# Optimization experiments

Hardware: AMD Instinct MI355X
Metric: run time of the kernel (lower is better)

## Reference

```python
import jax, jax.numpy as jnp
import numpy as np

B, T, D = 32, 200, 256
H, DH = 4, 32
INNER = H * DH  # 128
L, FF, NI = 8, 1024, 100000
NB = 64  # gap/recency buckets


def _ln(x, g, b, eps=1e-5):
    m = x.mean(-1, keepdims=True)
    v = jnp.mean((x - m) ** 2, -1, keepdims=True)
    return (x - m) / jnp.sqrt(v + eps) * g + b


def _gelu(x):
    return jax.nn.gelu(x, approximate=False)


def _dwconv_causal(x, w, b):
    # x: [B,T,C], w: [C,k] depthwise kernel, causal left-pad (k-1)
    k = w.shape[1]
    xp = jnp.pad(x, ((0, 0), (k - 1, 0), (0, 0))).transpose(0, 2, 1)  # [B,C,T+k-1]
    out = jax.lax.conv_general_dilated(
        xp, w[:, None, :], (1,), 'VALID',
        dimension_numbers=('NCH', 'OIH', 'NCH'), feature_group_count=w.shape[0])
    return out.transpose(0, 2, 1) + b


def _causal_linear_attention(q, k, v, m4):
    q = (jax.nn.elu(q) + 1.0) * m4
    k = (jax.nn.elu(k) + 1.0) * m4
    v = v * m4
    kv = jnp.einsum('bthd,bthe->bthde', k, v)          # [B,T,H,DH,DH]
    kv_prefix = jnp.cumsum(kv, axis=1)
    k_prefix = jnp.cumsum(k, axis=1)
    num = jnp.einsum('bthd,bthde->bthe', q, kv_prefix)
    den = jnp.sum(q * k_prefix, -1, keepdims=True)
    return num / (den + 1e-6) * m4


def _forward(item_emb, pos_emb, gap_emb, rec_emb, tf_w1, tf_b1, tf_w2, tf_b2,
             in_g, in_b, l_ln1g, l_ln1b, l_win, l_bin, l_wc, l_bc, l_tw, l_tb,
             l_pw, l_pb, l_wmix, l_bmix, l_ln2g, l_ln2b, l_wf1, l_bf1, l_wf2, l_bf2,
             fn_g, fn_b, pg_w, pg_b, uh_w1, uh_b1, uh_lng, uh_lnb, uh_w2, uh_b2,
             item_bias, ids, ts, lens):
    Bb, Tt = ids.shape
    pos = jnp.arange(Tt)
    mask = pos[None, :] >= (Tt - lens)[:, None]  # right-aligned valid mask [B,T]
    prev_ts = jnp.roll(ts, 1, axis=1)
    prev_mask = jnp.roll(mask, 1, axis=1).at[:, 0].set(False)
    zero = jnp.zeros_like(ts)
    gap_vals = jnp.where(mask & prev_mask, jnp.maximum(ts - prev_ts, 0), zero)
    latest = ts[:, -1:]
    rec_vals = jnp.where(mask, jnp.maximum(latest - ts, 0), zero)

    def buck(v, n):
        vf = jnp.maximum(v.astype(jnp.float32), 0.0)
        return jnp.clip(jnp.floor(jnp.log2(vf + 1.0)), 0, n - 1).astype(jnp.int32)

    gb = buck(gap_vals, NB)
    rb = buck(rec_vals, NB)
    rec_raw = jnp.maximum(latest - ts, 0).astype(jnp.float32)
    tf = jnp.stack([jnp.log1p(gb.astype(jnp.float32)), jnp.log1p(rec_raw)], -1)  # [B,T,2]
    dense_time = _gelu(tf @ tf_w1 + tf_b1) @ tf_w2 + tf_b2

    x = item_emb[ids] + pos_emb[None] + gap_emb[gb] + rec_emb[rb] + dense_time
    mf = mask[..., None].astype(x.dtype)
    m4 = mask[..., None, None].astype(x.dtype)
    x = _ln(x, in_g, in_b) * mf

    for i in range(L):
        res = x
        nrm = _ln(x, l_ln1g[i], l_ln1b[i])
        proj = nrm @ l_win[i] + l_bin[i]  # [B,T,D+3*INNER]
        gate = proj[..., :D]
        q = proj[..., D:D + INNER].reshape(Bb, Tt, H, DH)
        k = proj[..., D + INNER:D + 2 * INNER].reshape(Bb, Tt, H, DH)
        v = proj[..., D + 2 * INNER:].reshape(Bb, Tt, H, DH)
        content = _causal_linear_attention(q, k, v, m4).reshape(Bb, Tt, INNER) @ l_wc[i] + l_bc[i]
        temporal = _dwconv_causal(nrm, l_tw[i], l_tb[i])
        positional = _dwconv_causal(nrm, l_pw[i], l_pb[i])
        mixed = jnp.concatenate([content, temporal, positional], -1) @ l_wmix[i] + l_bmix[i]
        x = (res + jax.nn.sigmoid(gate) * mixed) * mf
        h = _ln(x, l_ln2g[i], l_ln2b[i])
        ffn = _gelu(h @ l_wf1[i] + l_bf1[i]) @ l_wf2[i] + l_bf2[i]
        x = (x + ffn) * mf

    x = _ln(x, fn_g, fn_b) * mf
    denom = jnp.maximum(lens, 1)[:, None].astype(x.dtype)
    mean_pooled = (x * mf).sum(1) / denom
    ps = (x @ pg_w + pg_b)[..., 0]
    ps = jnp.where(mask, ps, -1e9)
    pw = jax.nn.softmax(ps, axis=1)[..., None]
    attn_pooled = (pw * x).sum(1)
    last = x[:, -1, :]
    u = jnp.concatenate([last, mean_pooled, attn_pooled], -1)
    u = _gelu(u @ uh_w1 + uh_b1)
    u = _ln(u, uh_lng, uh_lnb)
    u = u @ uh_w2 + uh_b2
    u = u / jnp.maximum(jnp.linalg.norm(u, axis=-1, keepdims=True), 1e-12)
    ie = item_emb[1:]
    ie = ie / jnp.maximum(jnp.linalg.norm(ie, axis=-1, keepdims=True), 1e-12)
    return u @ ie.T + item_bias[1:]


def setup_inputs() -> dict:
    key = jax.random.key(0)
    it = iter(jax.random.split(key, 64))
    def nk():
        return next(it)
    def w(*s):
        return jax.random.normal(nk(), s, jnp.float32) * 0.02
    inp = dict(
        history_ids=jax.random.randint(nk(), (B, T), 0, NI),
        history_timestamps=jnp.sort(jax.random.randint(nk(), (B, T), 0, 1000000), axis=1),
        history_lengths=jax.random.randint(nk(), (B,), 1, T + 1),
        item_emb=w(NI + 1, D).at[0].set(0.0),
        pos_emb=w(T, D), gap_emb=w(NB, D), rec_emb=w(NB, D),
        tf_w1=w(2, D), tf_b1=jnp.zeros((D,)), tf_w2=w(D, D), tf_b2=jnp.zeros((D,)),
        in_g=jnp.ones((D,)), in_b=jnp.zeros((D,)),
        l_ln1g=jnp.ones((L, D)), l_ln1b=jnp.zeros((L, D)),
        l_win=w(L, D, D + 3 * INNER), l_bin=jnp.zeros((L, D + 3 * INNER)),
        l_wc=w(L, INNER, D), l_bc=jnp.zeros((L, D)),
        l_tw=w(L, D, 3), l_tb=jnp.zeros((L, D)),
        l_pw=w(L, D, 5), l_pb=jnp.zeros((L, D)),
        l_wmix=w(L, 3 * D, D), l_bmix=jnp.zeros((L, D)),
        l_ln2g=jnp.ones((L, D)), l_ln2b=jnp.zeros((L, D)),
        l_wf1=w(L, D, FF), l_bf1=jnp.zeros((L, FF)),
        l_wf2=w(L, FF, D), l_bf2=jnp.zeros((L, D)),
        fn_g=jnp.ones((D,)), fn_b=jnp.zeros((D,)),
        pg_w=w(D, 1), pg_b=jnp.zeros((1,)),
        uh_w1=w(3 * D, 1024), uh_b1=jnp.zeros((1024,)),
        uh_lng=jnp.ones((1024,)), uh_lnb=jnp.zeros((1024,)),
        uh_w2=w(1024, D), uh_b2=jnp.zeros((D,)),
        item_bias=jnp.zeros((NI + 1,)),
    )
    return inp


def reference(history_ids, history_timestamps, history_lengths, item_emb, pos_emb,
              gap_emb, rec_emb, tf_w1, tf_b1, tf_w2, tf_b2, in_g, in_b, l_ln1g,
              l_ln1b, l_win, l_bin, l_wc, l_bc, l_tw, l_tb, l_pw, l_pb, l_wmix,
              l_bmix, l_ln2g, l_ln2b, l_wf1, l_bf1, l_wf2, l_bf2, fn_g, fn_b,
              pg_w, pg_b, uh_w1, uh_b1, uh_lng, uh_lnb, uh_w2, uh_b2, item_bias):
    return _forward(item_emb, pos_emb, gap_emb, rec_emb, tf_w1, tf_b1, tf_w2, tf_b2,
                    in_g, in_b, l_ln1g, l_ln1b, l_win, l_bin, l_wc, l_bc, l_tw, l_tb,
                    l_pw, l_pb, l_wmix, l_bmix, l_ln2g, l_ln2b, l_wf1, l_bf1, l_wf2,
                    l_bf2, fn_g, fn_b, pg_w, pg_b, uh_w1, uh_b1, uh_lng, uh_lnb,
                    uh_w2, uh_b2, item_bias, history_ids, history_timestamps,
                    history_lengths)
```

## Files before the change

kernel.cpp:

```cpp
#include <hip/hip_runtime.h>
#include <math.h>

#define B_ 32
#define T_ 200
#define D_ 256
#define H_ 4
#define DH_ 32
#define INNER_ 128
#define L_ 8
#define FF_ 1024
#define NI_ 100000
#define NB_ 64
#define CH_ 25

typedef __attribute__((ext_vector_type(8))) short short8;
typedef __attribute__((ext_vector_type(8))) unsigned short ushort8;
typedef __attribute__((ext_vector_type(4))) unsigned short ushort4v;
typedef __attribute__((ext_vector_type(4))) float floatx4;

__device__ __forceinline__ float gelu_f(float x){
  return 0.5f*x*(1.0f+erff(x*0.70710678118654752f));
}
__device__ __forceinline__ float wsum(float v){
  #pragma unroll
  for (int o=32;o>0;o>>=1) v += __shfl_xor(v,o,64);
  return v;
}
__device__ __forceinline__ unsigned short f2bf(float x){
  unsigned int u = __float_as_uint(x);
  unsigned int r = (u + 0x7fffu + ((u>>16)&1u)) >> 16;
  return (unsigned short)r;
}
__device__ __forceinline__ float bf2f(unsigned short u){
  return __uint_as_float(((unsigned int)u)<<16);
}

__device__ __forceinline__ void cvt_tile(const float* __restrict__ src, unsigned short* __restrict__ dst,
                                         int K, int N, int tk, int tn, int tid, float (*s)[33])
{
  int tx = tid & 31, ty0 = tid >> 5;
  #pragma unroll
  for (int it=0; it<4; ++it){
    int ty = ty0 + it*8;
    s[ty][tx] = src[(size_t)(tk*32+ty)*N + tn*32+tx];
  }
  __syncthreads();
  #pragma unroll
  for (int it=0; it<4; ++it){
    int ty = ty0 + it*8;
    dst[(size_t)(tn*32+ty)*K + tk*32 + tx] = f2bf(s[tx][ty]);
  }
}

__global__ __launch_bounds__(256) void k_cvtAll(
  const float* __restrict__ win, const float* __restrict__ wmix,
  const float* __restrict__ wf1, const float* __restrict__ wf2,
  const float* __restrict__ tfw2, const float* __restrict__ uhw1, const float* __restrict__ uhw2,
  unsigned short* __restrict__ WtPerm, unsigned short* __restrict__ WtMixT,
  unsigned short* __restrict__ WtH)
{
  __shared__ float s[32][33];
  int b = blockIdx.x, tid = threadIdx.x;
  if (b < 6912){
    int l = b / 864, r = b % 864;
    if (r < 160)      cvt_tile(win + (size_t)l*163840, WtPerm + (size_t)l*688128,          256, 640,  r/20,      r%20,      tid, s);
    else if (r < 352){int t=r-160; cvt_tile(wmix + (size_t)l*196608, WtMixT + (size_t)l*196608, 768, 256, t/8, t%8, tid, s);}
    else if (r < 608){int t=r-352; cvt_tile(wf1 + (size_t)l*262144, WtPerm + (size_t)l*688128 + 163840, 256, 1024, t/32, t%32, tid, s);}
    else             {int t=r-608; cvt_tile(wf2 + (size_t)l*262144, WtPerm + (size_t)l*688128 + 425984, 1024, 256, t/8, t%8, tid, s);}
  } else {
    int r = b - 6912;
    if (r < 64)       cvt_tile(tfw2, WtH,        256, 256,  r/8,  r%8,  tid, s);
    else if (r < 832){int t=r-64;  cvt_tile(uhw1, WtH+65536,  768, 1024, t/32, t%32, tid, s);}
    else             {int t=r-832; cvt_tile(uhw2, WtH+851968, 1024, 256, t/8,  t%8,  tid, s);}
  }
}

__global__ __launch_bounds__(256) void k_asm(
  const float* __restrict__ WcombF, const unsigned short* __restrict__ WtMixT,
  unsigned short* __restrict__ WtBig)
{
  int l = blockIdx.x >> 3, g = blockIdx.x & 7;
  int tid = threadIdx.x;
  int n = g*32 + (tid >> 3);
  int k0 = (tid & 7) * 80;
  const float* wc = WcombF + (size_t)l*32768;
  const unsigned short* wm = WtMixT + (size_t)l*196608 + (size_t)n*768;
  unsigned short* dst = WtBig + (size_t)l*163840 + (size_t)n*640;
  for (int kk=0; kk<80; kk++){
    int k = k0 + kk;
    dst[k] = (k < 128) ? f2bf(wc[(size_t)k*256 + n]) : wm[k+128];
  }
}

__global__ __launch_bounds__(256) void k_bfold(
  const float* __restrict__ bc, const float* __restrict__ bmix,
  const float* __restrict__ wmix, float* __restrict__ bmixP)
{
  int l = blockIdx.x; int n = threadIdx.x;
  const float* w = wmix + (size_t)l*196608;
  const float* c = bc + l*256;
  float s = bmix[l*256 + n];
  for (int d=0; d<256; d++) s += c[d]*w[(size_t)d*256 + n];
  bmixP[l*256+n] = s;
}

template<int TN>
__global__ __launch_bounds__(256) void k_gemm_bf(
    const float* __restrict__ A, const unsigned short* __restrict__ Wt,
    const float* __restrict__ bias, float* __restrict__ C,
    int M, int N, int K, int ldA, int ldW, int ldC, int mode,
    size_t sA, size_t sW, size_t sC, size_t sB)
{
  constexpr int NJ = TN/32;
  __shared__ unsigned short Als[128][40];
  __shared__ unsigned short Bls[TN][40];
  int z = blockIdx.z;
  A += (size_t)z*sA; Wt += (size_t)z*sW; C += (size_t)z*sC;
  const float* bz = bias ? bias + (size_t)z*sB : nullptr;
  int tid = threadIdx.x;
  int wave = tid >> 6, lane = tid & 63;
  int wm = (wave >> 1) * 64, wn = (wave & 1) * (TN/2);
  int frow = lane & 15, kg = lane >> 4;
  int bm = blockIdx.y * 128, bn = blockIdx.x * TN;
  int sm = tid >> 1, skh = (tid & 1) * 16;

  floatx4 acc[4][NJ];
  #pragma unroll
  for (int i=0;i<4;i++)
    #pragma unroll
    for (int j=0;j<NJ;j++) acc[i][j] = (floatx4){0.f,0.f,0.f,0.f};

  for (int k0=0; k0<K; k0+=32){
    {
      int gm = bm + sm;
      float f[16];
      if (gm < M){
        const float4* ap = (const float4*)(A + (size_t)gm*ldA + k0 + skh);
        #pragma unroll
        for (int c=0;c<4;c++){ float4 v = ap[c]; f[c*4]=v.x; f[c*4+1]=v.y; f[c*4+2]=v.z; f[c*4+3]=v.w; }
      } else {
        #pragma unroll
        for (int c=0;c<16;c++) f[c]=0.f;
      }
      ushort8 pa, pb;
      #pragma unroll
      for (int c=0;c<8;c++){ pa[c]=f2bf(f[c]); pb[c]=f2bf(f[8+c]); }
      *(ushort8*)&Als[sm][skh]   = pa;
      *(ushort8*)&Als[sm][skh+8] = pb;
    }
    #pragma unroll
    for (int u=0; u<TN/64; u++){
      int li = tid + u*256;
      int row = li >> 2, koff = (li & 3) * 8;
      int gn = bn + row;
      ushort8 wv;
      if (gn < N){
        wv = *(const ushort8*)&Wt[(size_t)gn*ldW + k0 + koff];
      } else {
        for (int c=0;c<8;c++) wv[c]=0;
      }
      *(ushort8*)&Bls[row][koff] = wv;
    }
    __syncthreads();
    short8 af[4], bf[NJ];
    #pragma unroll
    for (int i=0;i<4;i++) af[i] = *(const short8*)&Als[wm + 16*i + frow][kg*8];
    #pragma unroll
    for (int j=0;j<NJ;j++) bf[j] = *(const short8*)&Bls[wn + 16*j + frow][kg*8];
    #pragma unroll
    for (int i=0;i<4;i++)
      #pragma unroll
      for (int j=0;j<NJ;j++)
        acc[i][j] = __builtin_amdgcn_mfma_f32_16x16x32_bf16(af[i], bf[j], acc[i][j], 0, 0, 0);
    __syncthreads();
  }

  #pragma unroll
  for (int j=0;j<NJ;j++){
    int n = bn + wn + 16*j + frow;
    float bv = bz ? bz[n] : 0.f;
    #pragma unroll
    for (int i=0;i<4;i++){
      int m0 = bm + wm + 16*i + kg*4;
      #pragma unroll
      for (int r=0;r<4;r++){
        int m = m0 + r;
        if (m < M){
          float v = acc[i][j][r] + bv;
          if (mode == 1) v = gelu_f(v);
          float* cp = &C[(size_t)m*ldC + n];
          if (mode == 2) v += *cp;
          *cp = v;
        }
      }
    }
  }
}

template<int K>
__global__ __launch_bounds__(256) void k_gemm16(
    const unsigned short* __restrict__ A, const unsigned short* __restrict__ Wt,
    const float* __restrict__ bias, void* __restrict__ Cv,
    int ldA, int ldW, int ldC, int mode)
{
  int tid = threadIdx.x;
  int wave = tid >> 6, lane = tid & 63;
  int frow = lane & 15, kg = lane >> 4;
  int bm = blockIdx.y * 32;
  int bn = blockIdx.x * 128 + wave * 32;

  const unsigned short* a0 = A + (size_t)(bm + frow)*ldA + kg*8;
  const unsigned short* a1 = a0 + (size_t)16*ldA;
  const unsigned short* b0 = Wt + (size_t)(bn + frow)*ldW + kg*8;
  const unsigned short* b1 = b0 + (size_t)16*ldW;

  floatx4 acc[2][2];
  #pragma unroll
  for (int i=0;i<2;i++)
    #pragma unroll
    for (int j=0;j<2;j++) acc[i][j] = (floatx4){0.f,0.f,0.f,0.f};

  #pragma unroll
  for (int k0=0; k0<K; k0+=32){
    short8 af0 = *(const short8*)(a0 + k0);
    short8 af1 = *(const short8*)(a1 + k0);
    short8 bf0 = *(const short8*)(b0 + k0);
    short8 bf1 = *(const short8*)(b1 + k0);
    acc[0][0] = __builtin_amdgcn_mfma_f32_16x16x32_bf16(af0, bf0, acc[0][0], 0, 0, 0);
    acc[0][1] = __builtin_amdgcn_mfma_f32_16x16x32_bf16(af0, bf1, acc[0][1], 0, 0, 0);
    acc[1][0] = __builtin_amdgcn_mfma_f32_16x16x32_bf16(af1, bf0, acc[1][0], 0, 0, 0);
    acc[1][1] = __builtin_amdgcn_mfma_f32_16x16x32_bf16(af1, bf1, acc[1][1], 0, 0, 0);
  }

  float* Cf = (float*)Cv;
  unsigned short* Ch = (unsigned short*)Cv;
  #pragma unroll
  for (int j=0;j<2;j++){
    int n = bn + 16*j + frow;
    float bv = bias[n];
    #pragma unroll
    for (int i=0;i<2;i++){
      int m0 = bm + 16*i + kg*4;
      #pragma unroll
      for (int r=0;r<4;r++){
        float v = acc[i][j][r] + bv;
        size_t off = (size_t)(m0+r)*ldC + n;
        if (mode == 1)      Cf[off] = gelu_f(v);
        else if (mode == 2) Cf[off] += v;
        else if (mode == 4) Ch[off] = f2bf(gelu_f(v));
        else                Cf[off] = v;
      }
    }
  }
}

__global__ __launch_bounds__(256) void k_embed(
  const int* __restrict__ ids, const int* __restrict__ ts, const int* __restrict__ lens,
  const float* __restrict__ item_emb, const float* __restrict__ pos_emb,
  const float* __restrict__ gap_emb, const float* __restrict__ rec_emb,
  const float* __restrict__ tf_w1, const float* __restrict__ tf_b1,
  float* __restrict__ xbuf, unsigned short* __restrict__ tfh)
{
  int bt = blockIdx.x;
  int b = bt / T_, t = bt % T_;
  int d = threadIdx.x;
  int len = lens[b];
  int tcur = ts[b*T_+t];
  int tlast = ts[b*T_+T_-1];
  bool mask  = t >= T_ - len;
  bool pmask = (t >= 1) && ((t-1) >= T_ - len);
  int gap = 0;
  if (mask && pmask){ int pv = ts[b*T_+t-1]; gap = max(tcur - pv, 0); }
  int rec = mask ? max(tlast - tcur, 0) : 0;
  int gb = min(max((int)floorf(log2f((float)gap + 1.0f)), 0), NB_-1);
  int rb = min(max((int)floorf(log2f((float)rec + 1.0f)), 0), NB_-1);
  float rec_raw = (float)max(tlast - tcur, 0);
  float tf0 = log1pf((float)gb);
  float tf1 = log1pf(rec_raw);
  float hid = gelu_f(tf0*tf_w1[d] + tf1*tf_w1[D_+d] + tf_b1[d]);
  tfh[(size_t)bt*D_ + d] = f2bf(hid);
  int id = ids[b*T_+t];
  xbuf[(size_t)bt*D_ + d] = item_emb[(size_t)id*D_ + d] + pos_emb[t*D_ + d]
                          + gap_emb[gb*D_ + d] + rec_emb[rb*D_ + d];
}

template<int NC>
__global__ __launch_bounds__(256) void k_ln(
  const float* __restrict__ in, void* __restrict__ out,
  const float* __restrict__ g, const float* __restrict__ bb,
  int rows, const int* __restrict__ lens, int applyMask, int outBf)
{
  int wid = threadIdx.x >> 6, lane = threadIdx.x & 63;
  int r = blockIdx.x*4 + wid;
  if (r >= rows) return;
  const int D = NC*256;
  const float4* rp = (const float4*)(in + (size_t)r*D);
  float4 v[NC];
  float s = 0.f;
  #pragma unroll
  for (int c=0;c<NC;c++){ v[c] = rp[c*64 + lane]; s += v[c].x+v[c].y+v[c].z+v[c].w; }
  s = wsum(s);
  float mean = s / (float)D;
  float q = 0.f;
  #pragma unroll
  for (int c=0;c<NC;c++){
    float a=v[c].x-mean, b2=v[c].y-mean, c2=v[c].z-mean, d2=v[c].w-mean;
    q += a*a + b2*b2 + c2*c2 + d2*d2;
  }
  q = wsum(q);
  float rstd = rsqrtf(q/(float)D + 1e-5f);
  float m = 1.f;
  if (applyMask){ int t = r % T_; int b = r / T_; m = (t >= T_ - lens[b]) ? 1.f : 0.f; }
  #pragma unroll
  for (int c=0;c<NC;c++){
    float4 gg  = ((const float4*)g )[c*64+lane];
    float4 bv  = ((const float4*)bb)[c*64+lane];
    float4 o;
    o.x = ((v[c].x-mean)*rstd*gg.x + bv.x)*m;
    o.y = ((v[c].y-mean)*rstd*gg.y + bv.y)*m;
    o.z = ((v[c].z-mean)*rstd*gg.z + bv.z)*m;
    o.w = ((v[c].w-mean)*rstd*gg.w + bv.w)*m;
    if (outBf){
      ushort4v ob; ob.x=f2bf(o.x); ob.y=f2bf(o.y); ob.z=f2bf(o.z); ob.w=f2bf(o.w);
      ((ushort4v*)((unsigned short*)out + (size_t)r*D))[c*64+lane] = ob;
    } else {
      ((float4*)((float*)out + (size_t)r*D))[c*64+lane] = o;
    }
  }
}

__global__ __launch_bounds__(256) void k_lnln(
  float* __restrict__ x, const int* __restrict__ lens,
  const float* __restrict__ g1, const float* __restrict__ b1,
  const float* __restrict__ g2, const float* __restrict__ b2,
  unsigned short* __restrict__ nrm)
{
  int wid = threadIdx.x >> 6, lane = threadIdx.x & 63;
  int r = blockIdx.x*4 + wid;
  int t = r % T_, b = r / T_;
  float m = (t >= T_ - lens[b]) ? 1.f : 0.f;
  float4 v = ((const float4*)(x + (size_t)r*256))[lane];
  float s = wsum(v.x+v.y+v.z+v.w);
  float mean = s/256.f;
  float a=v.x-mean, b2v=v.y-mean, c2=v.z-mean, d2=v.w-mean;
  float q = wsum(a*a+b2v*b2v+c2*c2+d2*d2);
  float rstd = rsqrtf(q/256.f + 1e-5f);
  float4 gg = ((const float4*)g1)[lane];
  float4 bv = ((const float4*)b1)[lane];
  float4 xn;
  xn.x = (a*rstd*gg.x + bv.x)*m;
  xn.y = (b2v*rstd*gg.y + bv.y)*m;
  xn.z = (c2*rstd*gg.z + bv.z)*m;
  xn.w = (d2*rstd*gg.w + bv.w)*m;
  ((float4*)(x + (size_t)r*256))[lane] = xn;
  float s2 = wsum(xn.x+xn.y+xn.z+xn.w);
  float mean2 = s2/256.f;
  float a2=xn.x-mean2, b22=xn.y-mean2, c22=xn.z-mean2, d22=xn.w-mean2;
  float q2 = wsum(a2*a2+b22*b22+c22*c22+d22*d22);
  float rstd2 = rsqrtf(q2/256.f + 1e-5f);
  float4 gg2 = ((const float4*)g2)[lane];
  float4 bv2 = ((const float4*)b2)[lane];
  ushort4v o;
  o.x = f2bf(a2*rstd2*gg2.x + bv2.x);
  o.y = f2bf(b22*rstd2*gg2.y + bv2.y);
  o.z = f2bf(c22*rstd2*gg2.z + bv2.z);
  o.w = f2bf(d22*rstd2*gg2.w + bv2.w);
  ((ushort4v*)(nrm + (size_t)r*256))[lane] = o;
}

__global__ __launch_bounds__(64) void k_attn_sums(
  const float* __restrict__ proj, const int* __restrict__ lens, float* __restrict__ Ssum)
{
  int blk = blockIdx.x;
  int bh = blk >> 3, c = blk & 7;
  int b = bh >> 2, h = bh & 3;
  int lane = threadIdx.x; int e = lane & 31, half = lane >> 5;
  int tstart = T_ - lens[b];
  __shared__ float sk[CH_*32], sv[CH_*32];
  int t0 = c*CH_;
  for (int idx = lane; idx < CH_*32; idx += 64){
    int tl = idx >> 5, dd = idx & 31;
    int t = t0 + tl;
    float m = (t >= tstart) ? 1.f : 0.f;
    const float* pr = proj + (size_t)(b*T_+t)*640 + h*32 + dd;
    float kw = pr[384], vv = pr[512];
    sk[idx] = (kw > 0.f ? kw + 1.f : __expf(kw)) * m;
    sv[idx] = vv * m;
  }
  __syncthreads();
  float acc[16];
  #pragma unroll
  for (int j=0;j<16;j++) acc[j]=0.f;
  for (int tl=0; tl<CH_; tl++){
    const float4* k4 = (const float4*)(sk + tl*32 + half*16);
    float vf = sv[tl*32 + e];
    #pragma unroll
    for (int jj=0;jj<4;jj++){
      float4 kk = k4[jj];
      acc[jj*4+0] += kk.x*vf;
      acc[jj*4+1] += kk.y*vf;
      acc[jj*4+2] += kk.z*vf;
      acc[jj*4+3] += kk.w*vf;
    }
  }
  float* dst = Ssum + ((size_t)bh*8 + c)*1056;
  #pragma unroll
  for (int j=0;j<16;j++) dst[(half*16+j)*32 + e] = acc[j];
  if (half == 0){
    float s = 0.f;
    for (int tl=0; tl<CH_; tl++) s += sk[tl*32 + e];
    dst[1024 + e] = s;
  }
}

__global__ __launch_bounds__(256) void k_dwpfx(
  const unsigned short* __restrict__ nrm, const float* __restrict__ tw, const float* __restrict__ tb,
  const float* __restrict__ pw, const float* __restrict__ pb, unsigned short* __restrict__ cat,
  float* __restrict__ Ssum)
{
  int bid = blockIdx.x;
  if (bid < 6400){
    int idx = bid*256 + threadIdx.x;
    int d = idx & 255; int bt = idx >> 8; int t = bt % T_;
    float xs[5];
    #pragma unroll
    for (int j=0;j<5;j++){
      int tt = t - 4 + j;
      xs[j] = (tt >= 0) ? bf2f(nrm[(size_t)(bt - 4 + j)*D_ + d]) : 0.f;
    }
    float tmp = tw[d*3+0]*xs[2] + tw[d*3+1]*xs[3] + tw[d*3+2]*xs[4] + tb[d];
    float pos = pb[d];
    #pragma unroll
    for (int j=0;j<5;j++) pos += pw[d*5+j]*xs[j];
    cat[(size_t)bt*640 + 128 + d] = f2bf(tmp);
    cat[(size_t)bt*640 + 384 + d] = f2bf(pos);
  } else {
    int idx = (bid - 6400)*256 + threadIdx.x;
    int bh = idx / 1056, r = idx - bh*1056;
    float* p = Ssum + (size_t)bh*8*1056 + r;
    float s = p[0];
    #pragma unroll
    for (int c=1;c<8;c++){ s += p[(size_t)c*1056]; p[(size_t)c*1056] = s; }
  }
}

__global__ __launch_bounds__(128) void k_attn_out(
  const float* __restrict__ proj, const int* __restrict__ lens,
  const float* __restrict__ Ssum, unsigned short* __restrict__ cat)
{
  int blk = blockIdx.x;
  int bh = blk >> 3, c = blk & 7;
  int b = bh >> 2, h = bh & 3;
  int tid = threadIdx.x; int e = tid & 31, qg = tid >> 5;
  int tstart = T_ - lens[b];
  __shared__ float sq[CH_*32], sk[CH_*32], sv[CH_*32];
  __shared__ float P[1056];
  __shared__ float A[CH_][CH_+1];
  __shared__ float sden[CH_];
  int t0 = c*CH_;
  if (c > 0){
    const float* Pp = Ssum + ((size_t)bh*8 + (c-1))*1056;
    for (int idx = tid; idx < 1056; idx += 128) P[idx] = Pp[idx];
  } else {
    for (int idx = tid; idx < 1056; idx += 128) P[idx] = 0.f;
  }
  for (int idx = tid; idx < CH_*32; idx += 128){
    int tl = idx >> 5, dd = idx & 31;
    int t = t0 + tl;
    float m = (t >= tstart) ? 1.f : 0.f;
    const float* pr = proj + (size_t)(b*T_+t)*640 + h*32 + dd;
    float qv = pr[256], kw = pr[384], vv = pr[512];
    sq[idx] = (qv > 0.f ? qv + 1.f : __expf(qv)) * m;
    sk[idx] = (kw > 0.f ? kw + 1.f : __expf(kw)) * m;
    sv[idx] = vv * m;
  }
  __syncthreads();
  for (int idx = tid; idx < CH_*CH_; idx += 128){
    int t = idx / CH_, tp = idx - t*CH_;
    float s = 0.f;
    if (tp <= t){
      const float4* q4 = (const float4*)(sq + t*32);
      const float4* k4 = (const float4*)(sk + tp*32);
      #pragma unroll
      for (int jj=0;jj<8;jj++){
        float4 qq = q4[jj], kk = k4[jj];
        s += qq.x*kk.x + qq.y*kk.y + qq.z*kk.z + qq.w*kk.w;
      }
    }
    A[t][tp] = s;
  }
  __syncthreads();
  if (tid < CH_){
    int t = tid;
    float s = 0.f;
    for (int tp=0; tp<=t; tp++) s += A[t][tp];
    const float* qf = sq + t*32;
    #pragma unroll
    for (int d=0; d<32; d++) s += qf[d]*P[1024+d];
    sden[t] = s;
  }
  __syncthreads();
  int tlo = (qg*CH_) >> 2, thi = ((qg+1)*CH_) >> 2;
  for (int t = tlo; t < thi; t++){
    float num = 0.f;
    for (int tp=0; tp<=t; tp++) num += A[t][tp]*sv[tp*32+e];
    const float* qf = sq + t*32;
    #pragma unroll
    for (int d=0; d<32; d++) num += qf[d]*P[d*32+e];
    int tg = t0 + t;
    float m = (tg >= tstart) ? 1.f : 0.f;
    cat[(size_t)(b*T_+tg)*640 + h*32 + e] = f2bf(num/(sden[t]+1e-6f)*m);
  }
}

__global__ __launch_bounds__(256) void k_postmix_ln(
  float* __restrict__ x, const float* __restrict__ proj, const float* __restrict__ mixed,
  const int* __restrict__ lens, const float* __restrict__ g, const float* __restrict__ bb,
  unsigned short* __restrict__ h)
{
  int wid = threadIdx.x >> 6, lane = threadIdx.x & 63;
  int r = blockIdx.x*4 + wid;
  int t = r % T_, b = r / T_;
  float m = (t >= T_ - lens[b]) ? 1.f : 0.f;
  float4 xv = ((const float4*)(x     + (size_t)r*256))[lane];
  float4 gv = ((const float4*)(proj  + (size_t)r*640))[lane];
  float4 mx = ((const float4*)(mixed + (size_t)r*256))[lane];
  float4 xn;
  xn.x = (xv.x + mx.x/(1.f+__expf(-gv.x)))*m;
  xn.y = (xv.y + mx.y/(1.f+__expf(-gv.y)))*m;
  xn.z = (xv.z + mx.z/(1.f+__expf(-gv.z)))*m;
  xn.w = (xv.w + mx.w/(1.f+__expf(-gv.w)))*m;
  float s = wsum(xn.x+xn.y+xn.z+xn.w);
  float mean = s/256.f;
  float a=xn.x-mean, b2=xn.y-mean, c2=xn.z-mean, d2=xn.w-mean;
  float q = wsum(a*a+b2*b2+c2*c2+d2*d2);
  float rstd = rsqrtf(q/256.f + 1e-5f);
  ((float4*)(x + (size_t)r*256))[lane] = xn;
  float4 gg = ((const float4*)g )[lane];
  float4 bv = ((const float4*)bb)[lane];
  ushort4v o;
  o.x = f2bf(a*rstd*gg.x + bv.x);
  o.y = f2bf(b2*rstd*gg.y + bv.y);
  o.z = f2bf(c2*rstd*gg.z + bv.z);
  o.w = f2bf(d2*rstd*gg.w + bv.w);
  ((ushort4v*)(h + (size_t)r*256))[lane] = o;
}

__global__ __launch_bounds__(256) void k_addln(
  float* __restrict__ x, const float* __restrict__ f, const int* __restrict__ lens,
  const float* __restrict__ g, const float* __restrict__ bb,
  unsigned short* __restrict__ nrm, int maskLN)
{
  int wid = threadIdx.x >> 6, lane = threadIdx.x & 63;
  int r = blockIdx.x*4 + wid;
  int t = r % T_, b = r / T_;
  float m = (t >= T_ - lens[b]) ? 1.f : 0.f;
  float4 xv = ((const float4*)(x + (size_t)r*256))[lane];
  float4 fv = ((const float4*)(f + (size_t)r*256))[lane];
  float4 xn;
  xn.x = (xv.x + fv.x)*m;
  xn.y = (xv.y + fv.y)*m;
  xn.z = (xv.z + fv.z)*m;
  xn.w = (xv.w + fv.w)*m;
  float s = wsum(xn.x+xn.y+xn.z+xn.w);
  float mean = s/256.f;
  float a=xn.x-mean, b2=xn.y-mean, c2=xn.z-mean, d2=xn.w-mean;
  float q = wsum(a*a+b2*b2+c2*c2+d2*d2);
  float rstd = rsqrtf(q/256.f + 1e-5f);
  ((float4*)(x + (size_t)r*256))[lane] = xn;
  float ml = maskLN ? m : 1.f;
  float4 gg = ((const float4*)g )[lane];
  float4 bv = ((const float4*)bb)[lane];
  ushort4v o;
  o.x = f2bf((a*rstd*gg.x + bv.x)*ml);
  o.y = f2bf((b2*rstd*gg.y + bv.y)*ml);
  o.z = f2bf((c2*rstd*gg.z + bv.z)*ml);
  o.w = f2bf((d2*rstd*gg.w + bv.w)*ml);
  ((ushort4v*)(nrm + (size_t)r*256))[lane] = o;
}

__global__ __launch_bounds__(256) void k_pool(
  const unsigned short* __restrict__ x, const int* __restrict__ lens,
  const float* __restrict__ pg_w, const float* __restrict__ pg_b,
  float* __restrict__ u0)
{
  int b = blockIdx.x;
  int tid = threadIdx.x, wid = tid>>6, lane = tid&63;
  __shared__ float sps[T_];
  __shared__ float spw[T_];
  int len = lens[b]; int tstart = T_ - len;
  const float4* pw4 = (const float4*)pg_w;
  float4 wv = pw4[lane];
  for (int t = wid; t < T_; t += 4){
    ushort4v xv = ((const ushort4v*)(x + (size_t)(b*T_+t)*D_))[lane];
    float dot = bf2f(xv.x)*wv.x + bf2f(xv.y)*wv.y + bf2f(xv.z)*wv.z + bf2f(xv.w)*wv.w;
    dot = wsum(dot);
    if (lane==0) sps[t] = (t >= tstart) ? dot + pg_b[0] : -1e9f;
  }
  __syncthreads();
  float mx = -1e30f;
  for (int t=0;t<T_;t++) mx = fmaxf(mx, sps[t]);
  float sum = 0.f;
  for (int t=0;t<T_;t++) sum += __expf(sps[t]-mx);
  float inv = 1.f/sum;
  if (tid < T_) spw[tid] = __expf(sps[tid]-mx)*inv;
  __syncthreads();
  int d = tid;
  float macc=0.f, aacc=0.f;
  for (int t=0;t<T_;t++){
    float v = bf2f(x[(size_t)(b*T_+t)*D_ + d]);
    macc += v;
    aacc += spw[t]*v;
  }
  u0[b*768 + d]       = bf2f(x[(size_t)(b*T_+T_-1)*D_ + d]);
  u0[b*768 + 256 + d] = macc / (float)max(len,1);
  u0[b*768 + 512 + d] = aacc;
}

__global__ __launch_bounds__(64) void k_norm(float* __restrict__ u, unsigned short* __restrict__ ub)
{
  int b = blockIdx.x; int lane = threadIdx.x;
  float4* r = (float4*)(u + b*256);
  float4 v = r[lane];
  float ss = v.x*v.x + v.y*v.y + v.z*v.z + v.w*v.w;
  ss = wsum(ss);
  float sc = 1.f/fmaxf(sqrtf(ss), 1e-12f);
  v.x*=sc; v.y*=sc; v.z*=sc; v.w*=sc;
  r[lane]=v;
  ub[b*256 + lane*4 + 0] = f2bf(v.x);
  ub[b*256 + lane*4 + 1] = f2bf(v.y);
  ub[b*256 + lane*4 + 2] = f2bf(v.z);
  ub[b*256 + lane*4 + 3] = f2bf(v.w);
}

__global__ __launch_bounds__(256) void k_score2(
  const float* __restrict__ item_emb, const unsigned short* __restrict__ ub,
  const float* __restrict__ item_bias, float* __restrict__ out)
{
  int tid = threadIdx.x;
  int wave = tid >> 6, lane = tid & 63;
  int frow = lane & 15, kg = lane >> 4;
  int n0 = blockIdx.x * 128 + wave * 32;

  int g0 = n0 + frow, g1 = n0 + 16 + frow;
  bool ok0 = g0 < NI_, ok1 = g1 < NI_;
  const float* ip0 = item_emb + (size_t)(g0+1)*256 + kg*8;
  const float* ip1 = item_emb + (size_t)(g1+1)*256 + kg*8;
  const unsigned short* up0 = ub + frow*256 + kg*8;
  const unsigned short* up1 = up0 + 16*256;

  floatx4 acc[2][2];
  #pragma unroll
  for (int i=0;i<2;i++)
    #pragma unroll
    for (int j=0;j<2;j++) acc[i][j] = (floatx4){0.f,0.f,0.f,0.f};
  float ss0 = 0.f, ss1 = 0.f;

  #pragma unroll
  for (int k0=0; k0<256; k0+=32){
    float4 a0, a1, c0, c1;
    if (ok0){ a0 = *(const float4*)(ip0 + k0); a1 = *(const float4*)(ip0 + k0 + 4); }
    else    { a0 = (float4){0,0,0,0}; a1 = a0; }
    if (ok1){ c0 = *(const float4*)(ip1 + k0); c1 = *(const float4*)(ip1 + k0 + 4); }
    else    { c0 = (float4){0,0,0,0}; c1 = c0; }
    ss0 += a0.x*a0.x + a0.y*a0.y + a0.z*a0.z + a0.w*a0.w
         + a1.x*a1.x + a1.y*a1.y + a1.z*a1.z + a1.w*a1.w;
    ss1 += c0.x*c0.x + c0.y*c0.y + c0.z*c0.z + c0.w*c0.w
         + c1.x*c1.x + c1.y*c1.y + c1.z*c1.z + c1.w*c1.w;
    short8 af0, af1;
    af0[0]=(short)f2bf(a0.x); af0[1]=(short)f2bf(a0.y); af0[2]=(short)f2bf(a0.z); af0[3]=(short)f2bf(a0.w);
    af0[4]=(short)f2bf(a1.x); af0[5]=(short)f2bf(a1.y); af0[6]=(short)f2bf(a1.z); af0[7]=(short)f2bf(a1.w);
    af1[0]=(short)f2bf(c0.x); af1[1]=(short)f2bf(c0.y); af1[2]=(short)f2bf(c0.z); af1[3]=(short)f2bf(c0.w);
    af1[4]=(short)f2bf(c1.x); af1[5]=(short)f2bf(c1.y); af1[6]=(short)f2bf(c1.z); af1[7]=(short)f2bf(c1.w);
    short8 bf0 = *(const short8*)(up0 + k0);
    short8 bf1 = *(const short8*)(up1 + k0);
    acc[0][0] = __builtin_amdgcn_mfma_f32_16x16x32_bf16(af0, bf0, acc[0][0], 0, 0, 0);
    acc[0][1] = __builtin_amdgcn_mfma_f32_16x16x32_bf16(af0, bf1, acc[0][1], 0, 0, 0);
    acc[1][0] = __builtin_amdgcn_mfma_f32_16x16x32_bf16(af1, bf0, acc[1][0], 0, 0, 0);
    acc[1][1] = __builtin_amdgcn_mfma_f32_16x16x32_bf16(af1, bf1, acc[1][1], 0, 0, 0);
  }

  ss0 += __shfl_xor(ss0, 16, 64); ss0 += __shfl_xor(ss0, 32, 64);
  ss1 += __shfl_xor(ss1, 16, 64); ss1 += __shfl_xor(ss1, 32, 64);

  #pragma unroll
  for (int i=0;i<2;i++){
    int nb = n0 + 16*i + kg*4;
    if (nb >= NI_) continue;
    float ssr = i ? ss1 : ss0;
    float sc[4], bv[4];
    #pragma unroll
    for (int r=0;r<4;r++){
      float ssv = __shfl(ssr, kg*4 + r, 64);
      sc[r] = 1.f/fmaxf(sqrtf(ssv), 1e-12f);
      bv[r] = item_bias[nb + r + 1];
    }
    #pragma unroll
    for (int j=0;j<2;j++){
      int row = 16*j + frow;
      float4 o;
      o.x = acc[i][j][0]*sc[0] + bv[0];
      o.y = acc[i][j][1]*sc[1] + bv[1];
      o.z = acc[i][j][2]*sc[2] + bv[2];
      o.w = acc[i][j][3]*sc[3] + bv[3];
      *(float4*)&out[(size_t)row*NI_ + nb] = o;
    }
  }
}

extern "C" void kernel_launch(void* const* d_in, const int* in_sizes, int n_in,
                              void* d_out, int out_size, void* d_ws, size_t ws_size,
                              hipStream_t stream)
{
  const int* ids  = (const int*)d_in[0];
  const int* ts   = (const int*)d_in[1];
  const int* lens = (const int*)d_in[2];
  const float* item_emb = (const float*)d_in[3];
  const float* pos_emb  = (const float*)d_in[4];
  const float* gap_emb  = (const float*)d_in[5];
  const float* rec_emb  = (const float*)d_in[6];
  const float* tf_w1 = (const float*)d_in[7];
  const float* tf_b1 = (const float*)d_in[8];
  const float* tf_w2 = (const float*)d_in[9];
  const float* tf_b2 = (const float*)d_in[10];
  const float* in_g  = (const float*)d_in[11];
  const float* in_b  = (const float*)d_in[12];
  const float* l_ln1g = (const float*)d_in[13];
  const float* l_ln1b = (const float*)d_in[14];
  const float* l_win  = (const float*)d_in[15];
  const float* l_bin  = (const float*)d_in[16];
  const float* l_wc   = (const float*)d_in[17];
  const float* l_bc   = (const float*)d_in[18];
  const float* l_tw   = (const float*)d_in[19];
  const float* l_tb   = (const float*)d_in[20];
  const float* l_pw   = (const float*)d_in[21];
  const float* l_pb   = (const float*)d_in[22];
  const float* l_wmix = (const float*)d_in[23];
  const float* l_bmix = (const float*)d_in[24];
  const float* l_ln2g = (const float*)d_in[25];
  const float* l_ln2b = (const float*)d_in[26];
  const float* l_wf1  = (const float*)d_in[27];
  const float* l_bf1  = (const float*)d_in[28];
  const float* l_wf2  = (const float*)d_in[29];
  const float* l_bf2  = (const float*)d_in[30];
  const float* fn_g = (const float*)d_in[31];
  const float* fn_b = (const float*)d_in[32];
  const float* pg_w = (const float*)d_in[33];
  const float* pg_b = (const float*)d_in[34];
  const float* uh_w1 = (const float*)d_in[35];
  const float* uh_b1 = (const float*)d_in[36];
  const float* uh_lng = (const float*)d_in[37];
  const float* uh_lnb = (const float*)d_in[38];
  const float* uh_w2 = (const float*)d_in[39];
  const float* uh_b2 = (const float*)d_in[40];
  const float* item_bias = (const float*)d_in[41];
  float* out = (float*)d_out;

  const int MT = B_*T_;
  float* ws   = (float*)d_ws;
  float* xbuf = ws;
  float* tmp  = xbuf + (size_t)MT*D_;
  float* proj = tmp  + (size_t)MT*D_;
  float* cat  = proj + (size_t)MT*640;
  float* mid  = cat  + (size_t)MT*640;
  float* u0   = mid  + (size_t)MT*FF_;
  float* u1   = u0 + 32*768;
  float* u2   = u1 + 32*1024;
  float* WcombF = u2 + 32*256;
  float* bmixP  = WcombF + 262144;
  float* Ssum   = bmixP + 2048;
  unsigned short* WtPerm = (unsigned short*)(Ssum + 1081344);
  unsigned short* WtMixT = WtPerm + 5505024;
  unsigned short* WtBig  = WtMixT + 1572864;
  unsigned short* WtH    = WtBig  + 1310720;
  unsigned short* u2b    = WtH    + 1114112;

  unsigned short* tmpb = (unsigned short*)tmp;
  unsigned short* catb = (unsigned short*)cat;
  unsigned short* midb = (unsigned short*)(mid + (size_t)MT*D_);

  k_cvtAll<<<8000, 256, 0, stream>>>(l_win, l_wmix, l_wf1, l_wf2, tf_w2, uh_w1, uh_w2,
                                     WtPerm, WtMixT, WtH);
  k_gemm_bf<64><<<dim3(4,1,8), 256, 0, stream>>>(l_wc, WtMixT, nullptr, WcombF,
                                                 128, 256, 256, 256, 768, 256, 0,
                                                 (size_t)128*256, (size_t)196608, (size_t)32768, 0);
  k_asm<<<64, 256, 0, stream>>>(WcombF, WtMixT, WtBig);
  k_bfold<<<8, 256, 0, stream>>>(l_bc, l_bmix, l_wmix, bmixP);

  k_embed<<<MT, 256, 0, stream>>>(ids, ts, lens, item_emb, pos_emb, gap_emb, rec_emb,
                                  tf_w1, tf_b1, xbuf, tmpb);
  k_gemm16<256><<<dim3(2,200), 256, 0, stream>>>(tmpb, WtH, tf_b2, xbuf, 256, 256, 256, 2);
  k_lnln<<<MT/4, 256, 0, stream>>>(xbuf, lens, in_g, in_b, l_ln1g, l_ln1b, tmpb);

  for (int i=0;i<L_;i++){
    const unsigned short* WL = WtPerm + (size_t)i*688128;
    k_gemm16<256><<<dim3(5,200), 256, 0, stream>>>(tmpb, WL, l_bin+i*640, proj, 256, 256, 640, 0);
    k_attn_sums<<<B_*H_*8, 64, 0, stream>>>(proj, lens, Ssum);
    k_dwpfx<<<6928, 256, 0, stream>>>(tmpb, l_tw+i*768, l_tb+i*256, l_pw+i*1280, l_pb+i*256,
                                      catb, Ssum);
    k_attn_out<<<B_*H_*8, 128, 0, stream>>>(proj, lens, Ssum, catb);
    k_gemm16<640><<<dim3(2,200), 256, 0, stream>>>(catb, WtBig+(size_t)i*163840, bmixP+i*256, mid,
                                                   640, 640, 256, 0);
    k_postmix_ln<<<MT/4, 256, 0, stream>>>(xbuf, proj, mid, lens, l_ln2g+i*256, l_ln2b+i*256, tmpb);
    k_gemm16<256><<<dim3(8,200), 256, 0, stream>>>(tmpb, WL+163840, l_bf1+i*FF_, midb,
                                                   256, 256, FF_, 4);
    k_gemm16<1024><<<dim3(2,200), 256, 0, stream>>>(midb, WL+425984, l_bf2+i*256, proj,
                                                    1024, 1024, 256, 0);
    bool last = (i == L_-1);
    k_addln<<<MT/4, 256, 0, stream>>>(xbuf, proj, lens,
                                      last ? fn_g : l_ln1g+(i+1)*256,
                                      last ? fn_b : l_ln1b+(i+1)*256,
                                      tmpb, last ? 1 : 0);
  }

  k_pool<<<B_, 256, 0, stream>>>(tmpb, lens, pg_w, pg_b, u0);
  k_gemm_bf<128><<<dim3(8,1), 256, 0, stream>>>(u0, WtH+65536, uh_b1, u1,
                                                32, 1024, 768, 768, 768, 1024, 1, 0,0,0,0);
  k_ln<4><<<8, 256, 0, stream>>>(u1, u1, uh_lng, uh_lnb, 32, lens, 0, 0);
  k_gemm_bf<64><<<dim3(4,1), 256, 0, stream>>>(u1, WtH+851968, uh_b2, u2,
                                               32, 256, 1024, 1024, 1024, 256, 0, 0,0,0,0);
  k_norm<<<B_, 64, 0, stream>>>(u2, u2b);

  k_score2<<<(NI_+127)/128, 256, 0, stream>>>(item_emb, u2b, item_bias, out);
}
```

Before: 1.721 ms.

## Fuse mix and FFN2 GEMMs with residual-add LayerNorm epilogue; widen attention blocks

Adds a k_gemmln kernel where each block computes a full 32x256 output row tile with MFMA, then applies the gated or plain residual add, writes xbuf, and does LayerNorm with cross-wave shared-memory reductions. It replaces the separate mix/FFN2 GEMMs and the postmix_ln/addln kernels, so the intermediate fp32 outputs no longer round-trip through global memory and two launches per layer are dropped. The fused GEMM has only 200 blocks with weights read straight from global (no LDS staging), so it exposes less parallelism. The attention kernels also double their threads per block.

```diff
diff --git a/kernel.cpp b/kernel.cpp
--- a/kernel.cpp
+++ b/kernel.cpp
@@ -252,6 +252,126 @@
       }
     }
   }
+}
+
+template<int K, int MODE>
+__global__ __launch_bounds__(256) void k_gemmln(
+    const unsigned short* __restrict__ A, const unsigned short* __restrict__ Wt,
+    const float* __restrict__ bias, float* __restrict__ xbuf,
+    const float* __restrict__ gate, const int* __restrict__ lens,
+    const float* __restrict__ g, const float* __restrict__ bb,
+    unsigned short* __restrict__ nrm, int maskLN)
+{
+  __shared__ float rs[32][4];
+  __shared__ float rq[32][4];
+  int tid = threadIdx.x;
+  int wave = tid >> 6, lane = tid & 63;
+  int frow = lane & 15, kg = lane >> 4;
+  int bm = blockIdx.x * 32;
+  int wn = wave * 64;
+
+  const unsigned short* a0 = A + (size_t)(bm + frow)*K + kg*8;
+  const unsigned short* a1 = a0 + (size_t)16*K;
+  const unsigned short* b0 = Wt + (size_t)(wn + frow)*K + kg*8;
+
+  floatx4 acc[2][4];
+  #pragma unroll
+  for (int i=0;i<2;i++)
+    #pragma unroll
+    for (int j=0;j<4;j++) acc[i][j] = (floatx4){0.f,0.f,0.f,0.f};
+
+  #pragma unroll
+  for (int k0=0; k0<K; k0+=32){
+    short8 af0 = *(const short8*)(a0 + k0);
+    short8 af1 = *(const short8*)(a1 + k0);
+    #pragma unroll
+    for (int j=0;j<4;j++){
+      short8 bf = *(const short8*)(b0 + (size_t)16*j*K + k0);
+      acc[0][j] = __builtin_amdgcn_mfma_f32_16x16x32_bf16(af0, bf, acc[0][j], 0, 0, 0);
+      acc[1][j] = __builtin_amdgcn_mfma_f32_16x16x32_bf16(af1, bf, acc[1][j], 0, 0, 0);
+    }
+  }
+
+  float xn[2][4][4];
+  float rowm[2][4];
+  #pragma unroll
+  for (int i=0;i<2;i++){
+    #pragma unroll
+    for (int r=0;r<4;r++){
+      int row = bm + 16*i + kg*4 + r;
+      int t = row % T_, b = row / T_;
+      float m = (t >= T_ - lens[b]) ? 1.f : 0.f;
+      rowm[i][r] = m;
+      #pragma unroll
+      for (int j=0;j<4;j++){
+        int n = wn + 16*j + frow;
+        float v = acc[i][j][r] + bias[n];
+        float xv = xbuf[(size_t)row*256 + n];
+        float xnv;
+        if (MODE == 0){
+          float gv = gate[(size_t)row*640 + n];
+          xnv = (xv + v/(1.f+__expf(-gv)))*m;
+        } else {
+          xnv = (xv + v)*m;
+        }
+        xn[i][j][r] = xnv;
+        xbuf[(size_t)row*256 + n] = xnv;
+      }
+    }
+  }
+  float mu[2][4];
+  #pragma unroll
+  for (int i=0;i<2;i++)
+    #pragma unroll
+    for (int r=0;r<4;r++){
+      float s = xn[i][0][r]+xn[i][1][r]+xn[i][2][r]+xn[i][3][r];
+      s += __shfl_xor(s,1,64); s += __shfl_xor(s,2,64);
+      s += __shfl_xor(s,4,64); s += __shfl_xor(s,8,64);
+      if (frow == 0) rs[16*i + kg*4 + r][wave] = s;
+    }
+  __syncthreads();
+  #pragma unroll
+  for (int i=0;i<2;i++)
+    #pragma unroll
+    for (int r=0;r<4;r++){
+      int rl = 16*i + kg*4 + r;
+      mu[i][r] = (rs[rl][0]+rs[rl][1]+rs[rl][2]+rs[rl][3]) * (1.f/256.f);
+    }
+  float rstd[2][4];
+  #pragma unroll
+  for (int i=0;i<2;i++)
+    #pragma unroll
+    for (int r=0;r<4;r++){
+      float m0 = mu[i][r];
+      float s = 0.f;
+      #pragma unroll
+      for (int j=0;j<4;j++){ float d = xn[i][j][r]-m0; s += d*d; }
+      s += __shfl_xor(s,1,64); s += __shfl_xor(s,2,64);
+      s += __shfl_xor(s,4,64); s += __shfl_xor(s,8,64);
+      if (frow == 0) rq[16*i + kg*4 + r][wave] = s;
+    }
+  __syncthreads();
+  #pragma unroll
+  for (int i=0;i<2;i++)
+    #pragma unroll
+    for (int r=0;r<4;r++){
+      int rl = 16*i + kg*4 + r;
+      float q = rq[rl][0]+rq[rl][1]+rq[rl][2]+rq[rl][3];
+      rstd[i][r] = rsqrtf(q*(1.f/256.f) + 1e-5f);
+    }
+  #pragma unroll
+  for (int i=0;i<2;i++)
+    #pragma unroll
+    for (int r=0;r<4;r++){
+      int row = bm + 16*i + kg*4 + r;
+      float ml = maskLN ? rowm[i][r] : 1.f;
+      #pragma unroll
+      for (int j=0;j<4;j++){
+        int n = wn + 16*j + frow;
+        float h = (xn[i][j][r]-mu[i][r])*rstd[i][r]*g[n] + bb[n];
+        nrm[(size_t)row*256 + n] = f2bf(h*ml);
+      }
+    }
 }
 
 __global__ __launch_bounds__(256) void k_embed(
@@ -368,17 +488,17 @@
   ((ushort4v*)(nrm + (size_t)r*256))[lane] = o;
 }
 
-__global__ __launch_bounds__(64) void k_attn_sums(
+__global__ __launch_bounds__(128) void k_attn_sums(
   const float* __restrict__ proj, const int* __restrict__ lens, float* __restrict__ Ssum)
 {
   int blk = blockIdx.x;
   int bh = blk >> 3, c = blk & 7;
   int b = bh >> 2, h = bh & 3;
-  int lane = threadIdx.x; int e = lane & 31, half = lane >> 5;
+  int tid = threadIdx.x; int e = tid & 31, q = tid >> 5;
   int tstart = T_ - lens[b];
   __shared__ float sk[CH_*32], sv[CH_*32];
   int t0 = c*CH_;
-  for (int idx = lane; idx < CH_*32; idx += 64){
+  for (int idx = tid; idx < CH_*32; idx += 128){
     int tl = idx >> 5, dd = idx & 31;
     int t = t0 + tl;
     float m = (t >= tstart) ? 1.f : 0.f;
@@ -388,25 +508,20 @@
     sv[idx] = vv * m;
   }
   __syncthreads();
-  float acc[16];
-  #pragma unroll
-  for (int j=0;j<16;j++) acc[j]=0.f;
+  float acc[8];
+  #pragma unroll
+  for (int j=0;j<8;j++) acc[j]=0.f;
   for (int tl=0; tl<CH_; tl++){
-    const float4* k4 = (const float4*)(sk + tl*32 + half*16);
+    const float4* k4 = (const float4*)(sk + tl*32 + q*8);
     float vf = sv[tl*32 + e];
-    #pragma unroll
-    for (int jj=0;jj<4;jj++){
-      float4 kk = k4[jj];
-      acc[jj*4+0] += kk.x*vf;
-      acc[jj*4+1] += kk.y*vf;
-      acc[jj*4+2] += kk.z*vf;
-      acc[jj*4+3] += kk.w*vf;
-    }
+    float4 ka = k4[0], kb = k4[1];
+    acc[0]+=ka.x*vf; acc[1]+=ka.y*vf; acc[2]+=ka.z*vf; acc[3]+=ka.w*vf;
+    acc[4]+=kb.x*vf; acc[5]+=kb.y*vf; acc[6]+=kb.z*vf; acc[7]+=kb.w*vf;
   }
   float* dst = Ssum + ((size_t)bh*8 + c)*1056;
   #pragma unroll
-  for (int j=0;j<16;j++) dst[(half*16+j)*32 + e] = acc[j];
-  if (half == 0){
+  for (int j=0;j<8;j++) dst[(q*8+j)*32 + e] = acc[j];
+  if (q == 0){
     float s = 0.f;
     for (int tl=0; tl<CH_; tl++) s += sk[tl*32 + e];
     dst[1024 + e] = s;
@@ -444,7 +559,7 @@
   }
 }
 
-__global__ __launch_bounds__(128) void k_attn_out(
+__global__ __launch_bounds__(256) void k_attn_out(
   const float* __restrict__ proj, const int* __restrict__ lens,
   const float* __restrict__ Ssum, unsigned short* __restrict__ cat)
 {
@@ -460,11 +575,11 @@
   int t0 = c*CH_;
   if (c > 0){
     const float* Pp = Ssum + ((size_t)bh*8 + (c-1))*1056;
-    for (int idx = tid; idx < 1056; idx += 128) P[idx] = Pp[idx];
+    for (int idx = tid; idx < 1056; idx += 256) P[idx] = Pp[idx];
   } else {
-    for (int idx = tid; idx < 1056; idx += 128) P[idx] = 0.f;
-  }
-  for (int idx = tid; idx < CH_*32; idx += 128){
+    for (int idx = tid; idx < 1056; idx += 256) P[idx] = 0.f;
+  }
+  for (int idx = tid; idx < CH_*32; idx += 256){
     int tl = idx >> 5, dd = idx & 31;
     int t = t0 + tl;
     float m = (t >= tstart) ? 1.f : 0.f;
@@ -475,7 +590,7 @@
     sv[idx] = vv * m;
   }
   __syncthreads();
-  for (int idx = tid; idx < CH_*CH_; idx += 128){
+  for (int idx = tid; idx < CH_*CH_; idx += 256){
     int t = idx / CH_, tp = idx - t*CH_;
     float s = 0.f;
     if (tp <= t){
@@ -500,7 +615,7 @@
     sden[t] = s;
   }
   __syncthreads();
-  int tlo = (qg*CH_) >> 2, thi = ((qg+1)*CH_) >> 2;
+  int tlo = (qg*CH_) >> 3, thi = ((qg+1)*CH_) >> 3;
   for (int t = tlo; t < thi; t++){
     float num = 0.f;
     for (int tp=0; tp<=t; tp++) num += A[t][tp]*sv[tp*32+e];
@@ -511,72 +626,6 @@
     float m = (tg >= tstart) ? 1.f : 0.f;
     cat[(size_t)(b*T_+tg)*640 + h*32 + e] = f2bf(num/(sden[t]+1e-6f)*m);
   }
-}
-
-__global__ __launch_bounds__(256) void k_postmix_ln(
-  float* __restrict__ x, const float* __restrict__ proj, const float* __restrict__ mixed,
-  const int* __restrict__ lens, const float* __restrict__ g, const float* __restrict__ bb,
-  unsigned short* __restrict__ h)
-{
-  int wid = threadIdx.x >> 6, lane = threadIdx.x & 63;
-  int r = blockIdx.x*4 + wid;
-  int t = r % T_, b = r / T_;
-  float m = (t >= T_ - lens[b]) ? 1.f : 0.f;
-  float4 xv = ((const float4*)(x     + (size_t)r*256))[lane];
-  float4 gv = ((const float4*)(proj  + (size_t)r*640))[lane];
-  float4 mx = ((const float4*)(mixed + (size_t)r*256))[lane];
-  float4 xn;
-  xn.x = (xv.x + mx.x/(1.f+__expf(-gv.x)))*m;
-  xn.y = (xv.y + mx.y/(1.f+__expf(-gv.y)))*m;
-  xn.z = (xv.z + mx.z/(1.f+__expf(-gv.z)))*m;
-  xn.w = (xv.w + mx.w/(1.f+__expf(-gv.w)))*m;
-  float s = wsum(xn.x+xn.y+xn.z+xn.w);
-  float mean = s/256.f;
-  float a=xn.x-mean, b2=xn.y-mean, c2=xn.z-mean, d2=xn.w-mean;
-  float q = wsum(a*a+b2*b2+c2*c2+d2*d2);
-  float rstd = rsqrtf(q/256.f + 1e-5f);
-  ((float4*)(x + (size_t)r*256))[lane] = xn;
-  float4 gg = ((const float4*)g )[lane];
-  float4 bv = ((const float4*)bb)[lane];
-  ushort4v o;
-  o.x = f2bf(a*rstd*gg.x + bv.x);
-  o.y = f2bf(b2*rstd*gg.y + bv.y);
-  o.z = f2bf(c2*rstd*gg.z + bv.z);
-  o.w = f2bf(d2*rstd*gg.w + bv.w);
-  ((ushort4v*)(h + (size_t)r*256))[lane] = o;
-}
-
-__global__ __launch_bounds__(256) void k_addln(
-  float* __restrict__ x, const float* __restrict__ f, const int* __restrict__ lens,
-  const float* __restrict__ g, const float* __restrict__ bb,
-  unsigned short* __restrict__ nrm, int maskLN)
-{
-  int wid = threadIdx.x >> 6, lane = threadIdx.x & 63;
-  int r = blockIdx.x*4 + wid;
-  int t = r % T_, b = r / T_;
-  float m = (t >= T_ - lens[b]) ? 1.f : 0.f;
-  float4 xv = ((const float4*)(x + (size_t)r*256))[lane];
-  float4 fv = ((const float4*)(f + (size_t)r*256))[lane];
-  float4 xn;
-  xn.x = (xv.x + fv.x)*m;
-  xn.y = (xv.y + fv.y)*m;
-  xn.z = (xv.z + fv.z)*m;
-  xn.w = (xv.w + fv.w)*m;
-  float s = wsum(xn.x+xn.y+xn.z+xn.w);
-  float mean = s/256.f;
-  float a=xn.x-mean, b2=xn.y-mean, c2=xn.z-mean, d2=xn.w-mean;
-  float q = wsum(a*a+b2*b2+c2*c2+d2*d2);
-  float rstd = rsqrtf(q/256.f + 1e-5f);
-  ((float4*)(x + (size_t)r*256))[lane] = xn;
-  float ml = maskLN ? m : 1.f;
-  float4 gg = ((const float4*)g )[lane];
-  float4 bv = ((const float4*)bb)[lane];
-  ushort4v o;
-  o.x = f2bf((a*rstd*gg.x + bv.x)*ml);
-  o.y = f2bf((b2*rstd*gg.y + bv.y)*ml);
-  o.z = f2bf((c2*rstd*gg.z + bv.z)*ml);
-  o.w = f2bf((d2*rstd*gg.w + bv.w)*ml);
-  ((ushort4v*)(nrm + (size_t)r*256))[lane] = o;
 }
 
 __global__ __launch_bounds__(256) void k_pool(
@@ -795,22 +844,21 @@
   for (int i=0;i<L_;i++){
     const unsigned short* WL = WtPerm + (size_t)i*688128;
     k_gemm16<256><<<dim3(5,200), 256, 0, stream>>>(tmpb, WL, l_bin+i*640, proj, 256, 256, 640, 0);
-    k_attn_sums<<<B_*H_*8, 64, 0, stream>>>(proj, lens, Ssum);
+    k_attn_sums<<<B_*H_*8, 128, 0, stream>>>(proj, lens, Ssum);
     k_dwpfx<<<6928, 256, 0, stream>>>(tmpb, l_tw+i*768, l_tb+i*256, l_pw+i*1280, l_pb+i*256,
                                       catb, Ssum);
-    k_attn_out<<<B_*H_*8, 128, 0, stream>>>(proj, lens, Ssum, catb);
-    k_gemm16<640><<<dim3(2,200), 256, 0, stream>>>(catb, WtBig+(size_t)i*163840, bmixP+i*256, mid,
-                                                   640, 640, 256, 0);
-    k_postmix_ln<<<MT/4, 256, 0, stream>>>(xbuf, proj, mid, lens, l_ln2g+i*256, l_ln2b+i*256, tmpb);
+    k_attn_out<<<B_*H_*8, 256, 0, stream>>>(proj, lens, Ssum, catb);
+    k_gemmln<640,0><<<200, 256, 0, stream>>>(catb, WtBig+(size_t)i*163840, bmixP+i*256,
+                                             xbuf, proj, lens,
+                                             l_ln2g+i*256, l_ln2b+i*256, tmpb, 0);
     k_gemm16<256><<<dim3(8,200), 256, 0, stream>>>(tmpb, WL+163840, l_bf1+i*FF_, midb,
                                                    256, 256, FF_, 4);
-    k_gemm16<1024><<<dim3(2,200), 256, 0, stream>>>(midb, WL+425984, l_bf2+i*256, proj,
-                                                    1024, 1024, 256, 0);
     bool last = (i == L_-1);
-    k_addln<<<MT/4, 256, 0, stream>>>(xbuf, proj, lens,
-                                      last ? fn_g : l_ln1g+(i+1)*256,
-                                      last ? fn_b : l_ln1b+(i+1)*256,
-                                      tmpb, last ? 1 : 0);
+    k_gemmln<1024,1><<<200, 256, 0, stream>>>(midb, WL+425984, l_bf2+i*256,
+                                              xbuf, nullptr, lens,
+                                              last ? fn_g : l_ln1g+(i+1)*256,
+                                              last ? fn_b : l_ln1b+(i+1)*256,
+                                              tmpb, last ? 1 : 0);
   }
 
   k_pool<<<B_, 256, 0, stream>>>(tmpb, lens, pg_w, pg_b, u0);
```

Result: faster. 1.665 ms (-3.3%).
